# Kernel optimization log

Hardware: AMD Instinct MI355X
Metric: run time of the kernel (lower is better)

## Reference

```python
import jax, jax.numpy as jnp
import numpy as np

B, S, H, NH, L = 8, 768, 768, 12, 12
W = 128          # one-sided window = attention_window // 2 (chunk_size=256)
D = H // NH      # head dim = 64
FF = 4 * H
EPS = 1e-12      # LongformerConfig layer_norm_eps
MAX_POS = 1024


def setup_inputs() -> dict:
    key = jax.random.key(0)
    ks = iter(jax.random.split(key, 64))
    rn = lambda shape, s=0.02: jax.random.normal(next(ks), shape, jnp.float32) * s
    inp = {
        "embedding": jax.random.normal(next(ks), (B, S, H), jnp.float32),
        "mask": jnp.ones((B, S), jnp.int32),  # unused by the original forward's core call
        "pos_emb": rn((MAX_POS, H)),
        "tte": rn((H,)),  # token_type embedding row 0 (token_type_ids are all zero)
        "emb_ln_g": jnp.ones((H,), jnp.float32),
        "emb_ln_b": jnp.zeros((H,), jnp.float32),
        "Wq": rn((L, H, H)), "bq": jnp.zeros((L, H), jnp.float32),
        "Wk": rn((L, H, H)), "bk": jnp.zeros((L, H), jnp.float32),
        "Wv": rn((L, H, H)), "bv": jnp.zeros((L, H), jnp.float32),
        "Wo": rn((L, H, H)), "bo": jnp.zeros((L, H), jnp.float32),
        "ln1_g": jnp.ones((L, H), jnp.float32), "ln1_b": jnp.zeros((L, H), jnp.float32),
        "Wi": rn((L, H, FF)), "bi": jnp.zeros((L, FF), jnp.float32),
        "Wo2": rn((L, FF, H)), "bo2": jnp.zeros((L, H), jnp.float32),
        "ln2_g": jnp.ones((L, H), jnp.float32), "ln2_b": jnp.zeros((L, H), jnp.float32),
        "gate_w": rn((H,)), "gate_b": jnp.zeros((), jnp.float32),
    }
    return inp


def layer_norm(x, g, b):
    mu = jnp.mean(x, axis=-1, keepdims=True)
    var = jnp.mean(jnp.square(x - mu), axis=-1, keepdims=True)
    return (x - mu) * jax.lax.rsqrt(var + EPS) * g + b


def sliding_window_attention(q, k, v):
    # q,k,v: [B,S,H]; each query attends to keys within +-W positions (band of 2W+1).
    n = S // W
    split = lambda x: x.reshape(B, S, NH, D).transpose(0, 2, 1, 3)  # [B,NH,S,D]
    qh = split(q) / np.sqrt(D)
    kh, vh = split(k), split(v)
    qc = qh.reshape(B, NH, n, W, D)

    def chunk3(x):
        # pad one chunk of zeros each side, gather [prev, cur, next] key chunks
        xp = jnp.pad(x, ((0, 0), (0, 0), (W, W), (0, 0))).reshape(B, NH, n + 2, W, D)
        return jnp.concatenate([xp[:, :, i:i + n] for i in range(3)], axis=3)  # [B,NH,n,3W,D]

    k3, v3 = chunk3(kh), chunk3(vh)
    scores = jnp.einsum('bhnqd,bhnkd->bhnqk', qc, k3)  # [B,NH,n,W,3W]

    qi = jnp.arange(W)[:, None]
    kj = jnp.arange(3 * W)[None, :]
    rel = kj - W - qi                                   # relative position j - i
    jglob = (jnp.arange(n)[:, None, None] - 1) * W + kj  # absolute key position
    valid = (jnp.abs(rel) <= W) & (jglob >= 0) & (jglob < S)  # [n,W,3W]

    scores = jnp.where(valid, scores, -1e9)
    p = jax.nn.softmax(scores, axis=-1)
    out = jnp.einsum('bhnqk,bhnkd->bhnqd', p, v3)
    return out.reshape(B, NH, S, D).transpose(0, 2, 1, 3).reshape(B, S, H)


def reference(embedding, mask, pos_emb, tte, emb_ln_g, emb_ln_b,
              Wq, bq, Wk, bk, Wv, bv, Wo, bo, ln1_g, ln1_b,
              Wi, bi, Wo2, bo2, ln2_g, ln2_b, gate_w, gate_b):
    # embeddings (position ids start at padding_idx+1 = 2, RoBERTa-style)
    pos_ids = jnp.arange(S) + 2
    x = embedding + pos_emb[pos_ids] + tte
    x = layer_norm(x, emb_ln_g, emb_ln_b)

    def layer(h, p):
        wq, b_q, wk, b_k, wv, b_v, wo, b_o, g1, be1, wi, b_i, wo2, b_o2, g2, be2 = p
        q = h @ wq + b_q
        k = h @ wk + b_k
        v = h @ wv + b_v
        a = sliding_window_attention(q, k, v)
        h = layer_norm(h + a @ wo + b_o, g1, be1)
        ff = jax.nn.gelu(h @ wi + b_i, approximate=False)
        h = layer_norm(h + ff @ wo2 + b_o2, g2, be2)
        return h, None

    x, _ = jax.lax.scan(layer, x, (Wq, bq, Wk, bk, Wv, bv, Wo, bo, ln1_g, ln1_b,
                                   Wi, bi, Wo2, bo2, ln2_g, ln2_b))
    gate = x @ gate_w + gate_b  # [B,S]
    return x, gate
```

## Files before the change

### kernel.cpp

```cpp
#include <hip/hip_runtime.h>
#include <hip/hip_bf16.h>
#include <math.h>
#include <stdint.h>

typedef __hip_bfloat16 bf16;
typedef __attribute__((ext_vector_type(8))) __bf16 bf16x8;
typedef __attribute__((ext_vector_type(4))) float f32x4;

#define HDIM 768
#define MROWS 6144
#define NCHUNK 6

__device__ __forceinline__ float bf2f(unsigned int u) {
  union { unsigned int i; float f; } c; c.i = u << 16; return c.f;
}

__device__ __forceinline__ void gload16(const void* g, void* l) {
  __builtin_amdgcn_global_load_lds((const __attribute__((address_space(1))) void*)g,
                                   (__attribute__((address_space(3))) void*)l, 16, 0, 0);
}

__device__ __forceinline__ float gelu_f(float v) {
  const float u2 = 1.5957691216057308f * (v + 0.044715f * v * v * v);
  const float e = __expf(u2);
  const float th = 1.f - 2.f / (e + 1.f);
  return 0.5f * v * (1.f + th);
}

__global__ __launch_bounds__(256) void wconv(
    const float* __restrict__ Wq, const float* __restrict__ Wk,
    const float* __restrict__ Wv, const float* __restrict__ Wo,
    const float* __restrict__ Wi, const float* __restrict__ Wo2,
    bf16* __restrict__ wt)
{
  __shared__ float tile[32][33];
  const int bid = blockIdx.x;
  const float* src; bf16* dst; int K, N, tIdx;
  if (bid < 2304) {
    int m = bid / 576; tIdx = bid % 576; K = 768; N = 768;
    src = (m == 0) ? Wq : (m == 1) ? Wk : (m == 2) ? Wv : Wo;
    dst = wt + (size_t)m * 589824;
  } else if (bid < 4608) {
    tIdx = bid - 2304; K = 768; N = 3072; src = Wi; dst = wt + 2359296;
  } else {
    tIdx = bid - 4608; K = 3072; N = 768; src = Wo2; dst = wt + 4718592;
  }
  const int tilesN = N >> 5;
  const int tn = tIdx % tilesN, tk = tIdx / tilesN;
  const int n0 = tn * 32, k0 = tk * 32;
  const int tx = threadIdx.x & 31, ty = threadIdx.x >> 5;
#pragma unroll
  for (int r = 0; r < 4; ++r)
    tile[ty + r * 8][tx] = src[(size_t)(k0 + ty + r * 8) * N + n0 + tx];
  __syncthreads();
#pragma unroll
  for (int r = 0; r < 4; ++r)
    dst[(size_t)(n0 + ty + r * 8) * K + k0 + tx] = __float2bfloat16(tile[tx][ty + r * 8]);
}

__global__ __launch_bounds__(256, 3) void gemm128(
    const bf16* __restrict__ A, const bf16* __restrict__ Bt,
    void* __restrict__ out, const float* __restrict__ b0,
    const float* __restrict__ b1, const float* __restrict__ b2,
    int gx, int N, int K, int NT, int epi, int nslice)
{
  __shared__ __align__(16) bf16 As[2][4096];
  __shared__ __align__(16) bf16 Bs[2][4096];

  const int nwg = gridDim.x;
  const int wg = blockIdx.x;
  const int L = (wg & 7) * (nwg >> 3) + (wg >> 3);
  const int per = nwg / nslice;
  const int slice = L / per;
  const int Lr = L - slice * per;
  const int bx = Lr % gx, by = Lr / gx;
  const int m0 = by * 128, n0 = bx * 128;
  const int kb0 = slice * (NT << 5);

  const int t = threadIdx.x;
  const int lane = t & 63;
  const int w = t >> 6;
  const int wr = w >> 1, wc = w & 1;
  const int fr = lane & 15;
  const int g = lane >> 4;

  f32x4 acc[4][4];
#pragma unroll
  for (int i = 0; i < 4; ++i)
#pragma unroll
    for (int j = 0; j < 4; ++j) acc[i][j] = (f32x4)0.f;

  const int r0 = t >> 2, q0 = t & 3;
  const int sq = q0 ^ ((r0 >> 1) & 3);
  const bf16* gA0 = A + (size_t)(m0 + r0) * K + kb0 + sq * 8;
  const bf16* gB0 = Bt + (size_t)(n0 + r0) * K + kb0 + sq * 8;
  const int dst0 = t * 16;

  unsigned offA[4], offB[4];
#pragma unroll
  for (int mf = 0; mf < 4; ++mf) {
    const int R = wr * 64 + mf * 16 + fr;
    offA[mf] = (unsigned)((R * 64 + g * 16) ^ (((R >> 1) & 3) << 4));
  }
#pragma unroll
  for (int nf = 0; nf < 4; ++nf) {
    const int R = wc * 64 + nf * 16 + fr;
    offB[nf] = (unsigned)((R * 64 + g * 16) ^ (((R >> 1) & 3) << 4));
  }
  const unsigned ldsA = (unsigned)(uintptr_t)&As[0][0];
  const unsigned ldsB = (unsigned)(uintptr_t)&Bs[0][0];

#define STAGE(KT, RB) {                                                    \
    const bf16* a_ = gA0 + (size_t)(KT) * 32;                              \
    const bf16* b_ = gB0 + (size_t)(KT) * 32;                              \
    gload16(a_,                  (char*)As[RB] + dst0);                    \
    gload16(a_ + (size_t)64 * K, (char*)As[RB] + dst0 + 4096);             \
    gload16(b_,                  (char*)Bs[RB] + dst0);                    \
    gload16(b_ + (size_t)64 * K, (char*)Bs[RB] + dst0 + 4096); }

  STAGE(0, 0)

#define ITER(KT, CUR) {                                                    \
    const int pf_ = ((KT) + 1 < NT) ? (KT) + 1 : (KT);                     \
    STAGE(pf_, (CUR) ^ 1)                                                  \
    asm volatile("s_waitcnt vmcnt(4)" ::: "memory");                       \
    __builtin_amdgcn_s_barrier();                                          \
    bf16x8 af[4], bfr[4];                                                  \
    const unsigned baA_ = ldsA + (CUR) * 8192u;                            \
    const unsigned baB_ = ldsB + (CUR) * 8192u;                            \
    _Pragma("unroll")                                                      \
    for (int mf = 0; mf < 4; ++mf)                                         \
      asm volatile("ds_read_b128 %0, %1" : "=v"(af[mf]) : "v"(baA_ + offA[mf])); \
    _Pragma("unroll")                                                      \
    for (int nf = 0; nf < 4; ++nf)                                         \
      asm volatile("ds_read_b128 %0, %1" : "=v"(bfr[nf]) : "v"(baB_ + offB[nf])); \
    asm volatile("s_waitcnt lgkmcnt(0)" ::: "memory");                     \
    __builtin_amdgcn_sched_barrier(0);                                     \
    __builtin_amdgcn_s_barrier();                                          \
    __builtin_amdgcn_s_setprio(1);                                         \
    _Pragma("unroll")                                                      \
    for (int mf = 0; mf < 4; ++mf)                                         \
      _Pragma("unroll")                                                    \
      for (int nf = 0; nf < 4; ++nf)                                       \
        acc[mf][nf] = __builtin_amdgcn_mfma_f32_16x16x32_bf16(af[mf], bfr[nf], acc[mf][nf], 0, 0, 0); \
    __builtin_amdgcn_s_setprio(0);                                         \
  }

#pragma unroll 1
  for (int kt = 0; kt < NT; kt += 2) {
    ITER(kt, 0)
    ITER(kt + 1, 1)
  }
  asm volatile("s_waitcnt vmcnt(0)" ::: "memory");
#undef ITER
#undef STAGE

  const int rr = (lane >> 4) * 4;
  const int cc0 = lane & 15;
  if (epi == 0) {
    const int mat = n0 / HDIM;
    const float* bias = (mat == 0) ? b0 : (mat == 1) ? b1 : b2;
    const float qs = (mat == 0) ? 0.125f : 1.0f;
    bf16* dst = (bf16*)out + (size_t)mat * MROWS * HDIM;
    const int nl = n0 - mat * HDIM;
#pragma unroll
    for (int mf = 0; mf < 4; ++mf)
#pragma unroll
      for (int nf = 0; nf < 4; ++nf) {
        const int row = m0 + wr * 64 + mf * 16 + rr;
        const int col = nl + wc * 64 + nf * 16 + cc0;
        const float bv = bias[col];
#pragma unroll
        for (int r = 0; r < 4; ++r)
          dst[(size_t)(row + r) * HDIM + col] = __float2bfloat16((acc[mf][nf][r] + bv) * qs);
      }
  } else if (epi == 2) {
    bf16* dst = (bf16*)out;
#pragma unroll
    for (int mf = 0; mf < 4; ++mf)
#pragma unroll
      for (int nf = 0; nf < 4; ++nf) {
        const int row = m0 + wr * 64 + mf * 16 + rr;
        const int col = n0 + wc * 64 + nf * 16 + cc0;
        const float bv = b0[col];
#pragma unroll
        for (int r = 0; r < 4; ++r)
          dst[(size_t)(row + r) * N + col] = __float2bfloat16(gelu_f(acc[mf][nf][r] + bv));
      }
  } else {
    bf16* dst = (bf16*)out + (size_t)slice * 4718592;
#pragma unroll
    for (int mf = 0; mf < 4; ++mf)
#pragma unroll
      for (int nf = 0; nf < 4; ++nf) {
        const int row = m0 + wr * 64 + mf * 16 + rr;
        const int col = n0 + wc * 64 + nf * 16 + cc0;
        const float bv = slice ? 0.f : b0[col];
#pragma unroll
        for (int r = 0; r < 4; ++r)
          dst[(size_t)(row + r) * N + col] = __float2bfloat16(acc[mf][nf][r] + bv);
      }
  }
}

__global__ __launch_bounds__(256) void attn_mfma(
    const bf16* __restrict__ qkv, bf16* __restrict__ attb)
{
  const int c = blockIdx.x, h = blockIdx.y, b = blockIdx.z;
  __shared__ unsigned int Vtw[64 * 64];
  __shared__ __align__(16) bf16 Pl[4][32 * 40];
  const int t = threadIdx.x;
  const int lane = t & 63;
  const int w = t >> 6;
  const int fr = lane & 15;
  const int g = lane >> 4;
  const bf16* Km = qkv + (size_t)4718592;
  const bf16* Vm = qkv + (size_t)9437184;
  const size_t qrow0 = (size_t)(b * 768 + c * 128);

  bf16x8 qf[2][2];
#pragma unroll
  for (int nt = 0; nt < 2; ++nt)
#pragma unroll
    for (int ks = 0; ks < 2; ++ks)
      qf[nt][ks] = *(const bf16x8*)(qkv + (qrow0 + w * 32 + nt * 16 + fr) * HDIM + h * 64 + ks * 32 + g * 8);

  f32x4 oacc[4][2];
#pragma unroll
  for (int i = 0; i < 4; ++i) { oacc[i][0] = (f32x4)0.f; oacc[i][1] = (f32x4)0.f; }
  float mrun[2] = {-1e30f, -1e30f};
  float lrun[2] = {0.f, 0.f};

#pragma unroll 1
  for (int cc = c - 1; cc <= c + 1; ++cc) {
    if (cc < 0 || cc >= NCHUNK) continue;
    __syncthreads();
    {
      const int d0 = (t & 7) * 8;
#pragma unroll
      for (int half = 0; half < 2; ++half) {
        const int kp2 = (t >> 3) + half * 32;
        const bf16* vr = Vm + ((size_t)(b * 768 + cc * 128) + kp2 * 2) * HDIM + h * 64 + d0;
        uint4 r0 = *(const uint4*)vr;
        uint4 r1 = *(const uint4*)(vr + HDIM);
        unsigned int a0[4] = {r0.x, r0.y, r0.z, r0.w};
        unsigned int a1[4] = {r1.x, r1.y, r1.z, r1.w};
#pragma unroll
        for (int e = 0; e < 8; ++e) {
          const int d = d0 + e;
          unsigned int lo = (a0[e >> 1] >> ((e & 1) * 16)) & 0xffffu;
          unsigned int hi = (a1[e >> 1] >> ((e & 1) * 16)) & 0xffffu;
          unsigned int byteoff = (unsigned int)(d * 256 + kp2 * 4);
          byteoff ^= ((((d >> 3) ^ d) & 7) << 4);
          Vtw[byteoff >> 2] = lo | (hi << 16);
        }
      }
    }
    __syncthreads();
    const int mode = (cc < c) ? 0 : (cc == c ? 1 : 2);
    const bf16* Kc = Km + ((size_t)(b * 768 + cc * 128)) * HDIM + h * 64;

#pragma unroll 1
    for (int kb = 0; kb < 4; ++kb) {
      f32x4 sacc[2][2];
      sacc[0][0] = sacc[0][1] = sacc[1][0] = sacc[1][1] = (f32x4)0.f;
#pragma unroll
      for (int ks = 0; ks < 2; ++ks)
#pragma unroll
        for (int mt = 0; mt < 2; ++mt) {
          bf16x8 kf = *(const bf16x8*)(Kc + (size_t)(kb * 32 + mt * 16 + fr) * HDIM + ks * 32 + g * 8);
          sacc[mt][0] = __builtin_amdgcn_mfma_f32_16x16x32_bf16(kf, qf[0][ks], sacc[mt][0], 0, 0, 0);
          sacc[mt][1] = __builtin_amdgcn_mfma_f32_16x16x32_bf16(kf, qf[1][ks], sacc[mt][1], 0, 0, 0);
        }
#pragma unroll
      for (int nt = 0; nt < 2; ++nt) {
        const int iq = w * 32 + nt * 16 + fr;
        float pm = -1e30f;
#pragma unroll
        for (int mt = 0; mt < 2; ++mt)
#pragma unroll
          for (int r = 0; r < 4; ++r) {
            const int j = kb * 32 + mt * 16 + g * 4 + r;
            const bool valid = (mode == 1) || (mode == 0 ? (j >= iq) : (j <= iq));
            const float sv = valid ? sacc[mt][nt][r] : -1e30f;
            sacc[mt][nt][r] = sv;
            pm = fmaxf(pm, sv);
          }
        pm = fmaxf(pm, __shfl_xor(pm, 16));
        pm = fmaxf(pm, __shfl_xor(pm, 32));
        const float mnew = fmaxf(fmaxf(mrun[nt], pm), -1e20f);
        const float sc = __expf(mrun[nt] - mnew);
        mrun[nt] = mnew;
        lrun[nt] *= sc;
#pragma unroll
        for (int mt = 0; mt < 4; ++mt) oacc[mt][nt] *= sc;
        float ps = 0.f;
#pragma unroll
        for (int mt = 0; mt < 2; ++mt) {
          union { bf16 hh[4]; uint2 uu; } pk;
#pragma unroll
          for (int r = 0; r < 4; ++r) {
            const float p = __expf(sacc[mt][nt][r] - mnew);
            ps += p;
            pk.hh[r] = __float2bfloat16(p);
          }
          *(uint2*)(&Pl[w][(nt * 16 + fr) * 40 + mt * 16 + g * 4]) = pk.uu;
        }
        ps += __shfl_xor(ps, 16);
        ps += __shfl_xor(ps, 32);
        lrun[nt] += ps;
      }
      bf16x8 bpf[2];
#pragma unroll
      for (int nt = 0; nt < 2; ++nt)
        bpf[nt] = *(const bf16x8*)(&Pl[w][(nt * 16 + fr) * 40 + g * 8]);
#pragma unroll
      for (int mt = 0; mt < 4; ++mt) {
        const int d = mt * 16 + fr;
        unsigned int byteoff = (unsigned int)(d * 256 + kb * 64 + g * 16);
        byteoff ^= ((((d >> 3) ^ d) & 7) << 4);
        bf16x8 vf = *(const bf16x8*)((const char*)Vtw + byteoff);
        oacc[mt][0] = __builtin_amdgcn_mfma_f32_16x16x32_bf16(vf, bpf[0], oacc[mt][0], 0, 0, 0);
        oacc[mt][1] = __builtin_amdgcn_mfma_f32_16x16x32_bf16(vf, bpf[1], oacc[mt][1], 0, 0, 0);
      }
    }
  }
#pragma unroll
  for (int nt = 0; nt < 2; ++nt) {
    const float rl = 1.f / lrun[nt];
    bf16* orow = attb + (qrow0 + w * 32 + nt * 16 + fr) * HDIM + h * 64;
#pragma unroll
    for (int mt = 0; mt < 4; ++mt) {
      union { bf16 hh[4]; uint2 uu; } ok;
#pragma unroll
      for (int r = 0; r < 4; ++r) ok.hh[r] = __float2bfloat16(oacc[mt][nt][r] * rl);
      *(uint2*)(orow + mt * 16 + g * 4) = ok.uu;
    }
  }
}

__device__ __forceinline__ void blk_reduce2(float& s1, float& s2) {
#pragma unroll
  for (int o = 32; o > 0; o >>= 1) { s1 += __shfl_xor(s1, o); s2 += __shfl_xor(s2, o); }
  __shared__ float red[8];
  const int w = threadIdx.x >> 6;
  if ((threadIdx.x & 63) == 0) { red[w] = s1; red[4 + w] = s2; }
  __syncthreads();
  s1 = red[0] + red[1] + red[2] + red[3];
  s2 = red[4] + red[5] + red[6] + red[7];
}

__global__ __launch_bounds__(256) void embed_ln(
    const float* __restrict__ emb, const float* __restrict__ pos,
    const float* __restrict__ tte, const float* __restrict__ g,
    const float* __restrict__ bt, float* __restrict__ x, bf16* __restrict__ xb)
{
  const int row = blockIdx.x;
  const int s = row % 768;
  const int t = threadIdx.x;
  const size_t base = (size_t)row * HDIM;
  const size_t pbase = (size_t)(s + 2) * HDIM;
  float v[3];
#pragma unroll
  for (int i = 0; i < 3; ++i) {
    const int idx = t + i * 256;
    v[i] = emb[base + idx] + pos[pbase + idx] + tte[idx];
  }
  float s1 = v[0] + v[1] + v[2];
  float s2 = v[0]*v[0] + v[1]*v[1] + v[2]*v[2];
  blk_reduce2(s1, s2);
  const float mu = s1 * (1.f / 768.f);
  const float var = s2 * (1.f / 768.f) - mu * mu;
  const float inv = rsqrtf(var + 1e-12f);
#pragma unroll
  for (int i = 0; i < 3; ++i) {
    const int idx = t + i * 256;
    const float o = (v[i] - mu) * inv * g[idx] + bt[idx];
    x[base + idx] = o;
    xb[base + idx] = __float2bfloat16(o);
  }
}

__global__ __launch_bounds__(256) void add_ln(
    const bf16* __restrict__ tmp, float* __restrict__ x, bf16* __restrict__ xb,
    const float* __restrict__ g, const float* __restrict__ bt)
{
  const int row = blockIdx.x;
  const int t = threadIdx.x;
  const size_t base = (size_t)row * HDIM;
  float v[3];
#pragma unroll
  for (int i = 0; i < 3; ++i) {
    const int idx = t + i * 256;
    v[i] = x[base + idx] + __bfloat162float(tmp[base + idx]);
  }
  float s1 = v[0] + v[1] + v[2];
  float s2 = v[0]*v[0] + v[1]*v[1] + v[2]*v[2];
  blk_reduce2(s1, s2);
  const float mu = s1 * (1.f / 768.f);
  const float var = s2 * (1.f / 768.f) - mu * mu;
  const float inv = rsqrtf(var + 1e-12f);
#pragma unroll
  for (int i = 0; i < 3; ++i) {
    const int idx = t + i * 256;
    const float o = (v[i] - mu) * inv * g[idx] + bt[idx];
    x[base + idx] = o;
    xb[base + idx] = __float2bfloat16(o);
  }
}

__global__ __launch_bounds__(256) void add_ln2(
    const bf16* __restrict__ tmp0, const bf16* __restrict__ tmp1,
    float* __restrict__ x, bf16* __restrict__ xb,
    const float* __restrict__ g, const float* __restrict__ bt)
{
  const int row = blockIdx.x;
  const int t = threadIdx.x;
  const size_t base = (size_t)row * HDIM;
  float v[3];
#pragma unroll
  for (int i = 0; i < 3; ++i) {
    const int idx = t + i * 256;
    v[i] = x[base + idx] + __bfloat162float(tmp0[base + idx]) + __bfloat162float(tmp1[base + idx]);
  }
  float s1 = v[0] + v[1] + v[2];
  float s2 = v[0]*v[0] + v[1]*v[1] + v[2]*v[2];
  blk_reduce2(s1, s2);
  const float mu = s1 * (1.f / 768.f);
  const float var = s2 * (1.f / 768.f) - mu * mu;
  const float inv = rsqrtf(var + 1e-12f);
#pragma unroll
  for (int i = 0; i < 3; ++i) {
    const int idx = t + i * 256;
    const float o = (v[i] - mu) * inv * g[idx] + bt[idx];
    x[base + idx] = o;
    xb[base + idx] = __float2bfloat16(o);
  }
}

__global__ __launch_bounds__(256) void gate_kernel(
    const float* __restrict__ x, const float* __restrict__ gw,
    const float* __restrict__ gb, float* __restrict__ out)
{
  const int row = blockIdx.x * 4 + (threadIdx.x >> 6);
  const int lane = threadIdx.x & 63;
  const float* xr = x + (size_t)row * HDIM;
  float s = 0.f;
#pragma unroll
  for (int i = 0; i < 12; ++i) s += xr[lane + i * 64] * gw[lane + i * 64];
#pragma unroll
  for (int o = 32; o > 0; o >>= 1) s += __shfl_xor(s, o);
  if (lane == 0) out[row] = s + gb[0];
}

extern "C" void kernel_launch(void* const* d_in, const int* in_sizes, int n_in,
                              void* d_out, int out_size, void* d_ws, size_t ws_size,
                              hipStream_t stream)
{
  const float* emb = (const float*)d_in[0];
  const float* pos = (const float*)d_in[2];
  const float* tte = (const float*)d_in[3];
  const float* eg  = (const float*)d_in[4];
  const float* eb  = (const float*)d_in[5];
  const float* Wq  = (const float*)d_in[6];
  const float* bq  = (const float*)d_in[7];
  const float* Wk  = (const float*)d_in[8];
  const float* bk  = (const float*)d_in[9];
  const float* Wv  = (const float*)d_in[10];
  const float* bv  = (const float*)d_in[11];
  const float* Wo  = (const float*)d_in[12];
  const float* bo  = (const float*)d_in[13];
  const float* g1  = (const float*)d_in[14];
  const float* be1 = (const float*)d_in[15];
  const float* Wi  = (const float*)d_in[16];
  const float* bi  = (const float*)d_in[17];
  const float* Wo2 = (const float*)d_in[18];
  const float* bo2 = (const float*)d_in[19];
  const float* g2  = (const float*)d_in[20];
  const float* be2 = (const float*)d_in[21];
  const float* gw  = (const float*)d_in[22];
  const float* gb  = (const float*)d_in[23];

  char* wsp = (char*)d_ws;
  bf16* wt   = (bf16*)wsp;
  bf16* xb   = (bf16*)(wsp + 14155776);
  bf16* qkvb = (bf16*)(wsp + 23592960);
  bf16* tmp  = (bf16*)(wsp + 61341696);
  bf16* attb = qkvb + (size_t)3 * 4718592;
  bf16* ffb  = qkvb;
  float* x   = (float*)d_out;
  float* gate = x + 4718592;

  embed_ln<<<6144, 256, 0, stream>>>(emb, pos, tte, eg, eb, x, xb);

  for (int l = 0; l < 12; ++l) {
    wconv<<<6912, 256, 0, stream>>>(Wq + (size_t)l * 589824, Wk + (size_t)l * 589824,
                                    Wv + (size_t)l * 589824, Wo + (size_t)l * 589824,
                                    Wi + (size_t)l * 2359296, Wo2 + (size_t)l * 2359296, wt);
    gemm128<<<864, 256, 0, stream>>>(xb, wt, qkvb,
        bq + l * 768, bk + l * 768, bv + l * 768, 18, 2304, 768, 24, 0, 1);
    attn_mfma<<<dim3(6, 12, 8), 256, 0, stream>>>(qkvb, attb);
    gemm128<<<288, 256, 0, stream>>>(attb, wt + 1769472, tmp,
        bo + l * 768, nullptr, nullptr, 6, 768, 768, 24, 3, 1);
    add_ln<<<6144, 256, 0, stream>>>(tmp, x, xb, g1 + l * 768, be1 + l * 768);
    gemm128<<<1152, 256, 0, stream>>>(xb, wt + 2359296, ffb,
        bi + l * 3072, nullptr, nullptr, 24, 3072, 768, 24, 2, 1);
    gemm128<<<576, 256, 0, stream>>>(ffb, wt + 4718592, tmp,
        bo2 + l * 768, nullptr, nullptr, 6, 768, 3072, 48, 3, 2);
    add_ln2<<<6144, 256, 0, stream>>>(tmp, tmp + 4718592, x, xb, g2 + l * 768, be2 + l * 768);
  }

  gate_kernel<<<1536, 256, 0, stream>>>(x, gw, gb, gate);
}
```

Baseline: 2.808 ms.

## Stage K into swizzled LDS and double-buffer K/V chunk loads in attention

The attention kernel now copies each key chunk into XOR-swizzled shared memory instead of reading K fragments straight from global memory. K and V use two LDS buffers, and the next chunk's loads are issued into registers before the current chunk's MFMA work so the global latency overlaps compute. The chunk loop drops the per-chunk skip branch, and the kb loop is fully unrolled. This costs more LDS (about 64KB per block) and more registers for prefetch, which may cut occupancy. The attention kernel is only a small part of the whole model's time.

After: 2.732 ms. -2.7%, faster.

```diff
diff --git a/kernel.cpp b/kernel.cpp
--- a/kernel.cpp
+++ b/kernel.cpp
@@ -207,7 +207,8 @@
     const bf16* __restrict__ qkv, bf16* __restrict__ attb)
 {
   const int c = blockIdx.x, h = blockIdx.y, b = blockIdx.z;
-  __shared__ unsigned int Vtw[64 * 64];
+  __shared__ __align__(16) bf16 Ks[2][8192];
+  __shared__ unsigned int Vtw[2][4096];
   __shared__ __align__(16) bf16 Pl[4][32 * 40];
   const int t = threadIdx.x;
   const int lane = t & 63;
@@ -231,36 +232,59 @@
   float mrun[2] = {-1e30f, -1e30f};
   float lrun[2] = {0.f, 0.f};
 
+  const int cc0 = (c > 0) ? c - 1 : 0;
+  const int nch = 1 + (c > 0) + (c < NCHUNK - 1);
+
+  uint4 kreg[4], vreg[4];
+
+#define KLOAD(CC) {                                                         \
+    const bf16* kp_ = Km + ((size_t)(b * 768 + (CC) * 128) + (t & 127)) * HDIM + h * 64 + (t >> 7) * 32; \
+    _Pragma("unroll")                                                       \
+    for (int j = 0; j < 4; ++j) kreg[j] = *(const uint4*)(kp_ + j * 8); }
+
+#define KWRITE(DB) {                                                        \
+    const int kr_ = t & 127, dh_ = t >> 7;                                  \
+    _Pragma("unroll")                                                       \
+    for (int j = 0; j < 4; ++j) {                                           \
+      const int s_ = (dh_ * 4 + j) ^ (kr_ & 7);                             \
+      *(uint4*)((char*)Ks[DB] + kr_ * 128 + s_ * 16) = kreg[j]; } }
+
+#define VLOAD(CC) {                                                         \
+    _Pragma("unroll")                                                       \
+    for (int half = 0; half < 2; ++half) {                                  \
+      const int kp2 = (t >> 3) + half * 32;                                 \
+      const bf16* vr_ = Vm + ((size_t)(b * 768 + (CC) * 128) + kp2 * 2) * HDIM + h * 64 + (t & 7) * 8; \
+      vreg[half * 2 + 0] = *(const uint4*)vr_;                              \
+      vreg[half * 2 + 1] = *(const uint4*)(vr_ + HDIM); } }
+
+#define VWRITE(DB) {                                                        \
+    const int d0_ = (t & 7) * 8;                                            \
+    _Pragma("unroll")                                                       \
+    for (int half = 0; half < 2; ++half) {                                  \
+      const int kp2 = (t >> 3) + half * 32;                                 \
+      unsigned int a0[4] = {vreg[half*2].x, vreg[half*2].y, vreg[half*2].z, vreg[half*2].w};      \
+      unsigned int a1[4] = {vreg[half*2+1].x, vreg[half*2+1].y, vreg[half*2+1].z, vreg[half*2+1].w}; \
+      _Pragma("unroll")                                                     \
+      for (int e = 0; e < 8; ++e) {                                         \
+        const int d = d0_ + e;                                              \
+        unsigned int lo = (a0[e >> 1] >> ((e & 1) * 16)) & 0xffffu;         \
+        unsigned int hi = (a1[e >> 1] >> ((e & 1) * 16)) & 0xffffu;         \
+        unsigned int byteoff = (unsigned int)(d * 256 + kp2 * 4);           \
+        byteoff ^= ((((d >> 3) ^ d) & 7) << 4);                             \
+        Vtw[DB][byteoff >> 2] = lo | (hi << 16); } } }
+
+  KLOAD(cc0) VLOAD(cc0)
+  KWRITE(0) VWRITE(0)
+  __syncthreads();
+
 #pragma unroll 1
-  for (int cc = c - 1; cc <= c + 1; ++cc) {
-    if (cc < 0 || cc >= NCHUNK) continue;
-    __syncthreads();
-    {
-      const int d0 = (t & 7) * 8;
-#pragma unroll
-      for (int half = 0; half < 2; ++half) {
-        const int kp2 = (t >> 3) + half * 32;
-        const bf16* vr = Vm + ((size_t)(b * 768 + cc * 128) + kp2 * 2) * HDIM + h * 64 + d0;
-        uint4 r0 = *(const uint4*)vr;
-        uint4 r1 = *(const uint4*)(vr + HDIM);
-        unsigned int a0[4] = {r0.x, r0.y, r0.z, r0.w};
-        unsigned int a1[4] = {r1.x, r1.y, r1.z, r1.w};
-#pragma unroll
-        for (int e = 0; e < 8; ++e) {
-          const int d = d0 + e;
-          unsigned int lo = (a0[e >> 1] >> ((e & 1) * 16)) & 0xffffu;
-          unsigned int hi = (a1[e >> 1] >> ((e & 1) * 16)) & 0xffffu;
-          unsigned int byteoff = (unsigned int)(d * 256 + kp2 * 4);
-          byteoff ^= ((((d >> 3) ^ d) & 7) << 4);
-          Vtw[byteoff >> 2] = lo | (hi << 16);
-        }
-      }
-    }
-    __syncthreads();
-    const int mode = (cc < c) ? 0 : (cc == c ? 1 : 2);
-    const bf16* Kc = Km + ((size_t)(b * 768 + cc * 128)) * HDIM + h * 64;
-
-#pragma unroll 1
+  for (int i = 0; i < nch; ++i) {
+    const int cur = i & 1;
+    const int ccc = cc0 + i;
+    if (i + 1 < nch) { KLOAD(cc0 + i + 1) VLOAD(cc0 + i + 1) }
+    const int mode = (ccc < c) ? 0 : ((ccc == c) ? 1 : 2);
+
+#pragma unroll
     for (int kb = 0; kb < 4; ++kb) {
       f32x4 sacc[2][2];
       sacc[0][0] = sacc[0][1] = sacc[1][0] = sacc[1][1] = (f32x4)0.f;
@@ -268,7 +292,9 @@
       for (int ks = 0; ks < 2; ++ks)
 #pragma unroll
         for (int mt = 0; mt < 2; ++mt) {
-          bf16x8 kf = *(const bf16x8*)(Kc + (size_t)(kb * 32 + mt * 16 + fr) * HDIM + ks * 32 + g * 8);
+          const int R = kb * 32 + mt * 16 + fr;
+          const int sl = (ks * 4 + g) ^ (R & 7);
+          bf16x8 kf = *(const bf16x8*)((const char*)Ks[cur] + R * 128 + sl * 16);
           sacc[mt][0] = __builtin_amdgcn_mfma_f32_16x16x32_bf16(kf, qf[0][ks], sacc[mt][0], 0, 0, 0);
           sacc[mt][1] = __builtin_amdgcn_mfma_f32_16x16x32_bf16(kf, qf[1][ks], sacc[mt][1], 0, 0, 0);
         }
@@ -319,12 +345,19 @@
         const int d = mt * 16 + fr;
         unsigned int byteoff = (unsigned int)(d * 256 + kb * 64 + g * 16);
         byteoff ^= ((((d >> 3) ^ d) & 7) << 4);
-        bf16x8 vf = *(const bf16x8*)((const char*)Vtw + byteoff);
+        bf16x8 vf = *(const bf16x8*)((const char*)Vtw[cur] + byteoff);
         oacc[mt][0] = __builtin_amdgcn_mfma_f32_16x16x32_bf16(vf, bpf[0], oacc[mt][0], 0, 0, 0);
         oacc[mt][1] = __builtin_amdgcn_mfma_f32_16x16x32_bf16(vf, bpf[1], oacc[mt][1], 0, 0, 0);
       }
     }
-  }
+    if (i + 1 < nch) { KWRITE(cur ^ 1) VWRITE(cur ^ 1) }
+    __syncthreads();
+  }
+#undef KLOAD
+#undef KWRITE
+#undef VLOAD
+#undef VWRITE
+
 #pragma unroll
   for (int nt = 0; nt < 2; ++nt) {
     const float rl = 1.f / lrun[nt];
```
